# Kernel optimization log

Measured on AMD Instinct MI355X. Metric: run time of the kernel, lower is better.

The kernel has to match this reference:

```python
import jax, jax.numpy as jnp
import numpy as np

H, C = 5, 64            # attention heads, per-head channels (out_channels=conv_dim)
NEG_SLOPE = 0.2         # GATv2 leaky_relu slope
N_NODES = 50000

def setup_inputs() -> dict:
    key = jax.random.key(0)
    ks = jax.random.split(key, 10)
    N, E = N_NODES, 400000
    node_dim, edge_dim = 128, 16
    s = 0.1
    return {
        'x': jax.random.normal(ks[0], (N, node_dim), jnp.float32),
        'edge_index': jax.random.randint(ks[1], (2, E), 0, N),
        'edge_attr': jax.random.normal(ks[2], (E, edge_dim), jnp.float32),
        'W0': jax.random.normal(ks[3], (node_dim, H * C), jnp.float32) * s,
        'b0': jnp.zeros((H * C,), jnp.float32),
        'We0': jax.random.normal(ks[4], (edge_dim, H * C), jnp.float32) * s,
        'att0': jax.random.normal(ks[5], (H, C), jnp.float32) * s,
        'bias0': jnp.zeros((C,), jnp.float32),
        'W12': jax.random.normal(ks[6], (2, C, H * C), jnp.float32) * s,
        'b12': jnp.zeros((2, H * C), jnp.float32),
        'We12': jax.random.normal(ks[7], (2, edge_dim, H * C), jnp.float32) * s,
        'att12': jax.random.normal(ks[8], (2, H, C), jnp.float32) * s,
        'bias12': jnp.zeros((2, C), jnp.float32),
    }

def _add_self_loops_mean(edge_index, edge_attr, N):
    # PyG add_self_loops(fill_value='mean'): self-loop attr = mean of incoming edge attrs per dst node
    dst = edge_index[1]
    sums = jax.ops.segment_sum(edge_attr, dst, num_segments=N)
    cnt = jax.ops.segment_sum(jnp.ones((edge_attr.shape[0], 1), edge_attr.dtype), dst, num_segments=N)
    loop_attr = sums / jnp.maximum(cnt, 1.0)
    loop = jnp.arange(N, dtype=edge_index.dtype)
    ei = jnp.concatenate([edge_index, jnp.stack([loop, loop])], axis=1)
    ea = jnp.concatenate([edge_attr, loop_attr], axis=0)
    return ei, ea

def _gatv2_layer(x, src, dst, eattr, W, b, We, att, bias, N):
    h = (x @ W + b).reshape(N, H, C)                     # shared lin_l==lin_r (share_weights=True)
    e = (eattr @ We).reshape(-1, H, C)                   # lin_edge (no bias)
    s = jax.nn.leaky_relu(h[src] + h[dst] + e, NEG_SLOPE)  # [E', H, C]
    logits = jnp.einsum('ehc,hc->eh', s, att)            # [E', H]
    m = jax.ops.segment_max(logits, dst, num_segments=N)
    m = jnp.where(jnp.isfinite(m), m, 0.0)
    ex = jnp.exp(logits - m[dst])
    denom = jax.ops.segment_sum(ex, dst, num_segments=N) + 1e-16
    alpha = ex / denom[dst]                              # per-dst softmax (dropout off: eval mode)
    msg = h[src] * alpha[:, :, None]
    out = jax.ops.segment_sum(msg, dst, num_segments=N)  # [N, H, C]
    return out.mean(axis=1) + bias                       # concat=False -> head mean, then bias

def reference(x, edge_index, edge_attr, W0, b0, We0, att0, bias0, W12, b12, We12, att12, bias12):
    N = x.shape[0]
    ei, ea = _add_self_loops_mean(edge_index, edge_attr, N)
    src, dst = ei[0], ei[1]
    h = jax.nn.elu(_gatv2_layer(x, src, dst, ea, W0, b0, We0, att0, bias0, N))
    for i in range(2):
        h = jax.nn.elu(_gatv2_layer(h, src, dst, ea, W12[i], b12[i], We12[i], att12[i], bias12[i], N))
    return h  # jk_mode='last'
```

## Files before the change

kernel.cpp:

```cpp
#include <hip/hip_runtime.h>
#include <hip/hip_fp16.h>
#include <math.h>

#define NH 5
#define NC 64
#define ED 16
#define HC 320
#define CH 32

typedef _Float16 h2  __attribute__((ext_vector_type(2)));
typedef _Float16 v8h __attribute__((ext_vector_type(8)));
typedef float    v4f __attribute__((ext_vector_type(4)));

template<int ctrl, int rmask>
__device__ __forceinline__ float dpp_add(float x) {
    int y = __builtin_amdgcn_update_dpp(0, __float_as_int(x), ctrl, rmask, 0xf, true);
    return x + __int_as_float(y);
}
__device__ __forceinline__ float wave_sum_all(float x) {
    x = dpp_add<0xb1, 0xf>(x);
    x = dpp_add<0x4e, 0xf>(x);
    x = dpp_add<0x114, 0xf>(x);
    x = dpp_add<0x118, 0xf>(x);
    x = dpp_add<0x142, 0xa>(x);
    x = dpp_add<0x143, 0xc>(x);
    return __int_as_float(__builtin_amdgcn_readlane(__float_as_int(x), 63));
}


__global__ void count_kernel(const int* __restrict__ dst, int* __restrict__ cnt, int E) {
    int t = blockIdx.x * blockDim.x + threadIdx.x;
    if (t >= E) return;
    atomicAdd(&cnt[dst[t]], 1);
}

__global__ void scan_kernel(const int* __restrict__ cnt, int* __restrict__ offsets,
                            int* __restrict__ cursor, int N) {
    __shared__ int sums[1024];
    int t = threadIdx.x;
    int chunk = (N + 1023) / 1024;
    int beg = t * chunk;
    int end = min(beg + chunk, N);
    int s = 0;
    for (int i = beg; i < end; ++i) s += cnt[i] + 1;
    sums[t] = s;
    __syncthreads();
    for (int o = 1; o < 1024; o <<= 1) {
        int v = (t >= o) ? sums[t - o] : 0;
        __syncthreads();
        sums[t] += v;
        __syncthreads();
    }
    int run = (t > 0) ? sums[t - 1] : 0;
    for (int i = beg; i < end; ++i) {
        offsets[i] = run; cursor[i] = run;
        run += cnt[i] + 1;
    }
    if (t == 0) offsets[N] = sums[1023];
}

__global__ void scatter_kernel(const int* __restrict__ src, const int* __restrict__ dst,
                               int* __restrict__ cursor, int2* __restrict__ recs, int N, int E) {
    int t = blockIdx.x * blockDim.x + threadIdx.x;
    if (t >= E + N) return;
    int d, s;
    if (t < E) { d = dst[t]; s = src[t]; }
    else       { d = t - E; s = t - E; }
    int pos = atomicAdd(&cursor[d], 1);
    recs[pos] = make_int2(s, t);
}

__global__ void loop_from_csr(const int* __restrict__ offsets, const int2* __restrict__ recs,
                              const float* __restrict__ ea, float* __restrict__ loop,
                              int N, int E) {
    int t = blockIdx.x * blockDim.x + threadIdx.x;
    int n = t >> 4, k = t & 15;
    if (n >= N) return;
    int beg = offsets[n], end = offsets[n + 1];
    float s = 0.f; int c = 0;
    for (int j = beg; j < end; ++j) {
        int y = recs[j].y;
        if (y < E) { s += ea[(size_t)y * ED + k]; ++c; }
    }
    loop[(size_t)n * ED + k] = s / (float)max(c, 1);
}

__global__ void reorder_ea(const int2* __restrict__ recs, const float* __restrict__ ea,
                           const float* __restrict__ loop, h2* __restrict__ easrt,
                           int* __restrict__ srcs, int R, int E) {
    int t = blockIdx.x * blockDim.x + threadIdx.x;
    int slot = t >> 3, k2 = t & 7;
    if (slot >= R) return;
    int2 rc = recs[slot];
    if (k2 == 0) srcs[slot] = rc.x;
    int y = rc.y;
    const float2* sp = (const float2*)((y < E) ? ea + (size_t)y * ED : loop + (size_t)(y - E) * ED);
    float2 f = sp[k2];
    h2 o; o.x = (_Float16)f.x; o.y = (_Float16)f.y;
    easrt[(size_t)slot * 8 + k2] = o;
}

__global__ void win_start_kernel(const int* __restrict__ offsets, int* __restrict__ winStart, int N) {
    int i = blockIdx.x * blockDim.x + threadIdx.x;
    if (i >= N) return;
    atomicMin(&winStart[offsets[i] / CH], i);
}

__global__ void cvt_f16(const float* __restrict__ in, _Float16* __restrict__ out, int n) {
    int i = blockIdx.x * blockDim.x + threadIdx.x;
    if (i < n) out[i] = (_Float16)in[i];
}

__global__ void transpose_w(const float* __restrict__ W, _Float16* __restrict__ Wt, int K) {
    int t = blockIdx.x * blockDim.x + threadIdx.x;
    if (t >= 320 * K) return;
    int k = t / 320, n = t % 320;
    Wt[(size_t)n * K + k] = (_Float16)W[t];
}

__global__ __launch_bounds__(256) void gemm_mfma(const _Float16* __restrict__ A,
                                                 const _Float16* __restrict__ Bt,
                                                 const float* __restrict__ bias,
                                                 _Float16* __restrict__ Cout, int M, int K) {
    int lane = threadIdx.x & 63;
    int wave = threadIdx.x >> 6;
    int m = lane & 15, quad = lane >> 4;
    int rowBase = (blockIdx.x * 4 + wave) * 16;
    if (rowBase >= M) return;

    v4f acc[20];
#pragma unroll
    for (int c = 0; c < 20; ++c) acc[c] = (v4f){0.f, 0.f, 0.f, 0.f};

    for (int k0 = 0; k0 < K; k0 += 32) {
        v8h a = *(const v8h*)&A[(size_t)(rowBase + m) * K + k0 + quad * 8];
#pragma unroll
        for (int c = 0; c < 20; ++c) {
            v8h b = *(const v8h*)&Bt[(size_t)(c * 16 + m) * K + k0 + quad * 8];
            acc[c] = __builtin_amdgcn_mfma_f32_16x16x32_f16(a, b, acc[c], 0, 0, 0);
        }
    }
    float bb[20];
#pragma unroll
    for (int c = 0; c < 20; ++c) bb[c] = bias[c * 16 + m];
#pragma unroll
    for (int r = 0; r < 4; ++r) {
        int row = rowBase + quad * 4 + r;
#pragma unroll
        for (int c03 = 0; c03 < 4; ++c03) {
            v8h o = {};
#pragma unroll
            for (int h = 0; h < NH; ++h) {
                int c = c03 + 4 * h;
                o[h] = (_Float16)(acc[c][r] + bb[c]);
            }
            *(v8h*)&Cout[(((size_t)row) * 64 + c03 * 16 + m) * 8] = o;
        }
    }
}

__global__ __launch_bounds__(256) void gat_fused(const _Float16* __restrict__ hbuf,
                                                 const int* __restrict__ offsets,
                                                 const int* __restrict__ srcs,
                                                 const h2* __restrict__ easrt,
                                                 const int* __restrict__ winStart,
                                                 const float* __restrict__ We,
                                                 const float* __restrict__ att,
                                                 const float* __restrict__ bias,
                                                 _Float16* __restrict__ outH,
                                                 float* __restrict__ outF,
                                                 int N, int R) {
    int lane = threadIdx.x & 63;
    int wave = (blockIdx.x * blockDim.x + threadIdx.x) >> 6;
    int totalWaves = (gridDim.x * blockDim.x) >> 6;
    const float L2E = 1.4426950408889634f;

    h2 we2[8 * NH];
#pragma unroll
    for (int k2 = 0; k2 < 8; ++k2)
#pragma unroll
        for (int h = 0; h < NH; ++h) {
            h2 w;
            w.x = (_Float16)We[(2 * k2) * HC + h * NC + lane];
            w.y = (_Float16)We[(2 * k2 + 1) * HC + h * NC + lane];
            we2[k2 * NH + h] = w;
        }
    float attc6[NH], attc4[NH];
#pragma unroll
    for (int h = 0; h < NH; ++h) {
        float a = att[h * NC + lane];
        attc6[h] = 0.6f * L2E * a;
        attc4[h] = 0.4f * L2E * a;
    }
    float bc = bias[lane];

    for (int w = wave; w * CH < R; w += totalWaves) {
        int i = winStart[w];
        if (i >= N) continue;
        int winEnd = w * CH + CH;
        for (; i < N; ++i) {
            int beg = offsets[i];
            if (beg >= winEnd) break;
            int end = offsets[i + 1];

            v8h hdv = *(const v8h*)&hbuf[((size_t)i * 64 + lane) * 8];
            float hd[NH];
#pragma unroll
            for (int h = 0; h < NH; ++h) hd[h] = (float)hdv[h];

            float l[NH] = {}, acc[NH] = {};
            int t = beg;
            for (; t + 2 <= end; t += 2) {
                int s0 = srcs[t], s1 = srcs[t + 1];
                v8h hs0v = *(const v8h*)&hbuf[((size_t)s0 * 64 + lane) * 8];
                v8h hs1v = *(const v8h*)&hbuf[((size_t)s1 * 64 + lane) * 8];
                const h2* ap = easrt + (size_t)t * 8;
                h2 a0[8], a1[8];
#pragma unroll
                for (int k2 = 0; k2 < 8; ++k2) { a0[k2] = ap[k2]; a1[k2] = ap[8 + k2]; }
                float hs0[NH], hs1[NH], p0[NH], p1[NH];
#pragma unroll
                for (int h = 0; h < NH; ++h) { hs0[h] = (float)hs0v[h]; hs1[h] = (float)hs1v[h]; }
#pragma unroll
                for (int h = 0; h < NH; ++h) {
                    float v0 = hs0[h] + hd[h];
                    float v1 = hs1[h] + hd[h];
#pragma unroll
                    for (int k2 = 0; k2 < 8; ++k2) {
                        v0 = __builtin_amdgcn_fdot2(a0[k2], we2[k2 * NH + h], v0, false);
                        v1 = __builtin_amdgcn_fdot2(a1[k2], we2[k2 * NH + h], v1, false);
                    }
                    p0[h] = fmaf(fabsf(v0), attc4[h], v0 * attc6[h]);
                    p1[h] = fmaf(fabsf(v1), attc4[h], v1 * attc6[h]);
                }
#pragma unroll
                for (int h = 0; h < NH; ++h) {
                    float pe0 = exp2f(wave_sum_all(p0[h]));
                    float pe1 = exp2f(wave_sum_all(p1[h]));
                    l[h] += pe0 + pe1;
                    acc[h] = fmaf(pe0, hs0[h], fmaf(pe1, hs1[h], acc[h]));
                }
            }
            if (t < end) {
                int s0 = srcs[t];
                v8h hs0v = *(const v8h*)&hbuf[((size_t)s0 * 64 + lane) * 8];
                const h2* ap = easrt + (size_t)t * 8;
                h2 a0[8];
#pragma unroll
                for (int k2 = 0; k2 < 8; ++k2) a0[k2] = ap[k2];
                float hs0[NH];
#pragma unroll
                for (int h = 0; h < NH; ++h) hs0[h] = (float)hs0v[h];
#pragma unroll
                for (int h = 0; h < NH; ++h) {
                    float v0 = hs0[h] + hd[h];
#pragma unroll
                    for (int k2 = 0; k2 < 8; ++k2)
                        v0 = __builtin_amdgcn_fdot2(a0[k2], we2[k2 * NH + h], v0, false);
                    float pe0 = exp2f(wave_sum_all(fmaf(fabsf(v0), attc4[h], v0 * attc6[h])));
                    l[h] += pe0;
                    acc[h] = fmaf(pe0, hs0[h], acc[h]);
                }
            }
            float o = 0.f;
#pragma unroll
            for (int h = 0; h < NH; ++h) o += acc[h] / l[h];
            o = o * 0.2f + bc;
            o = o > 0.f ? o : expm1f(o);
            if (outF) outF[(size_t)i * NC + lane] = o;
            else      outH[(size_t)i * NC + lane] = (_Float16)o;
        }
    }
}

extern "C" void kernel_launch(void* const* d_in, const int* in_sizes, int n_in,
                              void* d_out, int out_size, void* d_ws, size_t ws_size,
                              hipStream_t stream) {
    const float* x     = (const float*)d_in[0];
    const int*   ei    = (const int*)d_in[1];
    const float* ea    = (const float*)d_in[2];
    const float* W0    = (const float*)d_in[3];
    const float* b0    = (const float*)d_in[4];
    const float* We0   = (const float*)d_in[5];
    const float* att0  = (const float*)d_in[6];
    const float* bias0 = (const float*)d_in[7];
    const float* W12   = (const float*)d_in[8];
    const float* b12   = (const float*)d_in[9];
    const float* We12  = (const float*)d_in[10];
    const float* att12 = (const float*)d_in[11];
    const float* bias12= (const float*)d_in[12];

    int N = in_sizes[0] / 128;
    int E = in_sizes[1] / 2;
    int R = E + N;
    int numWin = (R + CH - 1) / CH;
    const int* srcArr = ei;
    const int* dstArr = ei + E;

    char* ws = (char*)d_ws;
    size_t off = 0;
    auto alloc = [&](size_t bytes) -> void* {
        void* p = ws + off;
        off = (off + bytes + 255) & ~(size_t)255;
        return p;
    };
    int*      cnt     = (int*)alloc((size_t)N * 4);
    int*      offsets = (int*)alloc((size_t)(N + 1) * 4);
    int*      cursor  = (int*)alloc((size_t)N * 4);
    int2*     recs    = (int2*)alloc((size_t)R * 8);
    float*    loop    = (float*)alloc((size_t)N * ED * 4);
    _Float16* hbuf    = (_Float16*)alloc((size_t)N * 64 * 8 * 2);
    _Float16* acth    = (_Float16*)alloc((size_t)N * NC * 2);
    _Float16* xh      = (_Float16*)alloc((size_t)N * 128 * 2);
    _Float16* Wth0    = (_Float16*)alloc((size_t)320 * 128 * 2);
    _Float16* Wth1    = (_Float16*)alloc((size_t)320 * 64 * 2);
    _Float16* Wth2    = (_Float16*)alloc((size_t)320 * 64 * 2);
    int*      winStart= (int*)alloc((size_t)(numWin + 1) * 4);
    h2*       easrt   = (h2*)alloc((size_t)R * 32);
    int*      srcs    = (int*)alloc((size_t)R * 4);

    (void)hipMemsetAsync(cnt, 0, (size_t)N * 4, stream);
    (void)hipMemsetAsync(winStart, 0x7f, (size_t)(numWin + 1) * 4, stream);
    count_kernel<<<(E + 255) / 256, 256, 0, stream>>>(dstArr, cnt, E);
    scan_kernel<<<1, 1024, 0, stream>>>(cnt, offsets, cursor, N);
    scatter_kernel<<<(E + N + 255) / 256, 256, 0, stream>>>(srcArr, dstArr, cursor, recs, N, E);
    loop_from_csr<<<((size_t)N * ED + 255) / 256, 256, 0, stream>>>(offsets, recs, ea, loop, N, E);
    reorder_ea<<<((size_t)R * 8 + 255) / 256, 256, 0, stream>>>(recs, ea, loop, easrt, srcs, R, E);
    win_start_kernel<<<(N + 255) / 256, 256, 0, stream>>>(offsets, winStart, N);
    cvt_f16<<<((size_t)N * 128 + 255) / 256, 256, 0, stream>>>(x, xh, N * 128);
    transpose_w<<<(320 * 128 + 255) / 256, 256, 0, stream>>>(W0, Wth0, 128);
    transpose_w<<<(320 * 64 + 255) / 256, 256, 0, stream>>>(W12, Wth1, 64);
    transpose_w<<<(320 * 64 + 255) / 256, 256, 0, stream>>>(W12 + 64 * HC, Wth2, 64);

    float* dout = (float*)d_out;
    int gemmBlocks = (N / 16 + 3) / 4 + 1;
    int fusedBlocks = (numWin + 3) / 4;

    const _Float16* As[3]  = {xh, acth, acth};
    const _Float16* Bts[3] = {Wth0, Wth1, Wth2};
    int Ks[3] = {128, 64, 64};
    const float* bs[3]   = {b0, b12, b12 + HC};
    const float* Wes[3]  = {We0, We12, We12 + ED * HC};
    const float* atts[3] = {att0, att12, att12 + NH * NC};
    const float* bis[3]  = {bias0, bias12, bias12 + NC};
    for (int layer = 0; layer < 3; ++layer) {
        gemm_mfma<<<gemmBlocks, 256, 0, stream>>>(As[layer], Bts[layer], bs[layer], hbuf, N, Ks[layer]);
        gat_fused<<<fusedBlocks, 256, 0, stream>>>(hbuf, offsets, srcs, easrt, winStart,
                                                   Wes[layer], atts[layer], bis[layer],
                                                   acth, (layer == 2) ? dout : nullptr, N, R);
    }
}
```

Baseline: 890.5 us.

## Split padded 8-head node buffer into 4-head vector plus separate fifth-head array

The per-node projected features were stored padded to 8 halves per channel (16 bytes) even though only 5 heads are used. They are now split into a 4-head vec4 array plus a separate single-half array for the fifth head, which cuts the bytes gathered per source edge from 16 to 10. The cost is two load instructions per gather instead of one, touching two separate cache lines. The wave reduction is also rewritten as inline-asm DPP adds, so the compiler can no longer schedule or combine those instructions.

```diff
diff --git a/kernel.cpp b/kernel.cpp
--- a/kernel.cpp
+++ b/kernel.cpp
@@ -9,21 +9,23 @@
 #define CH 32
 
 typedef _Float16 h2  __attribute__((ext_vector_type(2)));
+typedef _Float16 v4h __attribute__((ext_vector_type(4)));
 typedef _Float16 v8h __attribute__((ext_vector_type(8)));
 typedef float    v4f __attribute__((ext_vector_type(4)));
 
-template<int ctrl, int rmask>
-__device__ __forceinline__ float dpp_add(float x) {
-    int y = __builtin_amdgcn_update_dpp(0, __float_as_int(x), ctrl, rmask, 0xf, true);
-    return x + __int_as_float(y);
-}
 __device__ __forceinline__ float wave_sum_all(float x) {
-    x = dpp_add<0xb1, 0xf>(x);
-    x = dpp_add<0x4e, 0xf>(x);
-    x = dpp_add<0x114, 0xf>(x);
-    x = dpp_add<0x118, 0xf>(x);
-    x = dpp_add<0x142, 0xa>(x);
-    x = dpp_add<0x143, 0xc>(x);
+    asm("v_add_f32_dpp %0, %1, %0 quad_perm:[1,0,3,2] row_mask:0xf bank_mask:0xf"
+        : "+v"(x) : "v"(x));
+    asm("v_add_f32_dpp %0, %1, %0 quad_perm:[2,3,0,1] row_mask:0xf bank_mask:0xf"
+        : "+v"(x) : "v"(x));
+    asm("v_add_f32_dpp %0, %1, %0 row_half_mirror row_mask:0xf bank_mask:0xf"
+        : "+v"(x) : "v"(x));
+    asm("v_add_f32_dpp %0, %1, %0 row_mirror row_mask:0xf bank_mask:0xf"
+        : "+v"(x) : "v"(x));
+    asm("v_add_f32_dpp %0, %1, %0 row_bcast:15 row_mask:0xa bank_mask:0xf"
+        : "+v"(x) : "v"(x));
+    asm("v_add_f32_dpp %0, %1, %0 row_bcast:31 row_mask:0xc bank_mask:0xf"
+        : "+v"(x) : "v"(x));
     return __int_as_float(__builtin_amdgcn_readlane(__float_as_int(x), 63));
 }
 
@@ -121,7 +123,8 @@
 __global__ __launch_bounds__(256) void gemm_mfma(const _Float16* __restrict__ A,
                                                  const _Float16* __restrict__ Bt,
                                                  const float* __restrict__ bias,
-                                                 _Float16* __restrict__ Cout, int M, int K) {
+                                                 _Float16* __restrict__ CoutA,
+                                                 _Float16* __restrict__ CoutB, int M, int K) {
     int lane = threadIdx.x & 63;
     int wave = threadIdx.x >> 6;
     int m = lane & 15, quad = lane >> 4;
@@ -148,18 +151,22 @@
         int row = rowBase + quad * 4 + r;
 #pragma unroll
         for (int c03 = 0; c03 < 4; ++c03) {
-            v8h o = {};
-#pragma unroll
-            for (int h = 0; h < NH; ++h) {
+            v4h o;
+#pragma unroll
+            for (int h = 0; h < 4; ++h) {
                 int c = c03 + 4 * h;
                 o[h] = (_Float16)(acc[c][r] + bb[c]);
             }
-            *(v8h*)&Cout[(((size_t)row) * 64 + c03 * 16 + m) * 8] = o;
+            int cw = c03 * 16 + m;
+            *(v4h*)&CoutA[(((size_t)row) * 64 + cw) * 4] = o;
+            int c4 = c03 + 16;
+            CoutB[((size_t)row) * 64 + cw] = (_Float16)(acc[c4][r] + bb[c4]);
         }
     }
 }
 
-__global__ __launch_bounds__(256) void gat_fused(const _Float16* __restrict__ hbuf,
+__global__ __launch_bounds__(256) void gat_fused(const _Float16* __restrict__ hA,
+                                                 const _Float16* __restrict__ hB,
                                                  const int* __restrict__ offsets,
                                                  const int* __restrict__ srcs,
                                                  const h2* __restrict__ easrt,
@@ -203,24 +210,28 @@
             if (beg >= winEnd) break;
             int end = offsets[i + 1];
 
-            v8h hdv = *(const v8h*)&hbuf[((size_t)i * 64 + lane) * 8];
+            v4h hd4 = *(const v4h*)&hA[((size_t)i * 64 + lane) * 4];
             float hd[NH];
 #pragma unroll
-            for (int h = 0; h < NH; ++h) hd[h] = (float)hdv[h];
+            for (int h = 0; h < 4; ++h) hd[h] = (float)hd4[h];
+            hd[4] = (float)hB[(size_t)i * 64 + lane];
 
             float l[NH] = {}, acc[NH] = {};
             int t = beg;
             for (; t + 2 <= end; t += 2) {
                 int s0 = srcs[t], s1 = srcs[t + 1];
-                v8h hs0v = *(const v8h*)&hbuf[((size_t)s0 * 64 + lane) * 8];
-                v8h hs1v = *(const v8h*)&hbuf[((size_t)s1 * 64 + lane) * 8];
+                v4h hs0v = *(const v4h*)&hA[((size_t)s0 * 64 + lane) * 4];
+                v4h hs1v = *(const v4h*)&hA[((size_t)s1 * 64 + lane) * 4];
+                _Float16 hs0e = hB[(size_t)s0 * 64 + lane];
+                _Float16 hs1e = hB[(size_t)s1 * 64 + lane];
                 const h2* ap = easrt + (size_t)t * 8;
                 h2 a0[8], a1[8];
 #pragma unroll
                 for (int k2 = 0; k2 < 8; ++k2) { a0[k2] = ap[k2]; a1[k2] = ap[8 + k2]; }
                 float hs0[NH], hs1[NH], p0[NH], p1[NH];
 #pragma unroll
-                for (int h = 0; h < NH; ++h) { hs0[h] = (float)hs0v[h]; hs1[h] = (float)hs1v[h]; }
+                for (int h = 0; h < 4; ++h) { hs0[h] = (float)hs0v[h]; hs1[h] = (float)hs1v[h]; }
+                hs0[4] = (float)hs0e; hs1[4] = (float)hs1e;
 #pragma unroll
                 for (int h = 0; h < NH; ++h) {
                     float v0 = hs0[h] + hd[h];
@@ -243,14 +254,16 @@
             }
             if (t < end) {
                 int s0 = srcs[t];
-                v8h hs0v = *(const v8h*)&hbuf[((size_t)s0 * 64 + lane) * 8];
+                v4h hs0v = *(const v4h*)&hA[((size_t)s0 * 64 + lane) * 4];
+                _Float16 hs0e = hB[(size_t)s0 * 64 + lane];
                 const h2* ap = easrt + (size_t)t * 8;
                 h2 a0[8];
 #pragma unroll
                 for (int k2 = 0; k2 < 8; ++k2) a0[k2] = ap[k2];
                 float hs0[NH];
 #pragma unroll
-                for (int h = 0; h < NH; ++h) hs0[h] = (float)hs0v[h];
+                for (int h = 0; h < 4; ++h) hs0[h] = (float)hs0v[h];
+                hs0[4] = (float)hs0e;
 #pragma unroll
                 for (int h = 0; h < NH; ++h) {
                     float v0 = hs0[h] + hd[h];
@@ -309,7 +322,8 @@
     int*      cursor  = (int*)alloc((size_t)N * 4);
     int2*     recs    = (int2*)alloc((size_t)R * 8);
     float*    loop    = (float*)alloc((size_t)N * ED * 4);
-    _Float16* hbuf    = (_Float16*)alloc((size_t)N * 64 * 8 * 2);
+    _Float16* hbufA   = (_Float16*)alloc((size_t)N * 64 * 4 * 2);
+    _Float16* hbufB   = (_Float16*)alloc((size_t)N * 64 * 2);
     _Float16* acth    = (_Float16*)alloc((size_t)N * NC * 2);
     _Float16* xh      = (_Float16*)alloc((size_t)N * 128 * 2);
     _Float16* Wth0    = (_Float16*)alloc((size_t)320 * 128 * 2);
@@ -344,8 +358,9 @@
     const float* atts[3] = {att0, att12, att12 + NH * NC};
     const float* bis[3]  = {bias0, bias12, bias12 + NC};
     for (int layer = 0; layer < 3; ++layer) {
-        gemm_mfma<<<gemmBlocks, 256, 0, stream>>>(As[layer], Bts[layer], bs[layer], hbuf, N, Ks[layer]);
-        gat_fused<<<fusedBlocks, 256, 0, stream>>>(hbuf, offsets, srcs, easrt, winStart,
+        gemm_mfma<<<gemmBlocks, 256, 0, stream>>>(As[layer], Bts[layer], bs[layer],
+                                                  hbufA, hbufB, N, Ks[layer]);
+        gat_fused<<<fusedBlocks, 256, 0, stream>>>(hbufA, hbufB, offsets, srcs, easrt, winStart,
                                                    Wes[layer], atts[layer], bis[layer],
                                                    acth, (layer == 2) ? dout : nullptr, N, R);
     }
```

Result: faster. 851.2 us (-4.4%).
